# Kernel optimization log

Hardware: AMD Instinct MI355X
Metric: run time of the kernel (lower is better)

Reference implementation:

```python
import jax, jax.numpy as jnp
import numpy as np

H = 256
V = 10000
E = 300000


def setup_inputs() -> dict:
    key = jax.random.key(0)
    ks = jax.random.split(key, 7)
    s = 1.0 / np.sqrt(H)  # torch nn.Linear default init scale
    x = jax.random.normal(ks[0], (V, H), dtype=jnp.float32)
    e = jax.random.normal(ks[1], (E, H), dtype=jnp.float32)
    edge_index = jax.random.randint(ks[2], (2, E), 0, V, dtype=jnp.int64)
    Us_w = jax.random.uniform(ks[3], (H, H), dtype=jnp.float32, minval=-s, maxval=s)
    Us_b = jax.random.uniform(ks[4], (H,), dtype=jnp.float32, minval=-s, maxval=s)
    Vs_w = jax.random.uniform(ks[5], (H, H), dtype=jnp.float32, minval=-s, maxval=s)
    Vs_b = jax.random.uniform(ks[6], (H,), dtype=jnp.float32, minval=-s, maxval=s)
    return {"x": x, "e": e, "edge_index": edge_index,
            "Us_w": Us_w, "Us_b": Us_b, "Vs_w": Vs_w, "Vs_b": Vs_b}


def reference(x, e, edge_index, Us_w, Us_b, Vs_w, Vs_b):
    # Ue = Us(e): (E, H); Vx = Vs(x): (V, H)  [torch Linear: y = x @ W.T + b]
    Ue = jnp.einsum('eh,oh->eo', e, Us_w) + Us_b
    Vx = jnp.einsum('vh,oh->vo', x, Vs_w) + Vs_b
    src, dst = edge_index[0], edge_index[1]
    # gather + add epilogue: e_new = Ue + Vx[src] + Vx[dst]
    e_new = Ue + Vx[src] + Vx[dst]
    return e_new
```

## Files before the change

kernel.cpp:

```cpp
#include <hip/hip_runtime.h>


typedef __bf16 bf16_t;
typedef __bf16 bf16x4 __attribute__((ext_vector_type(4)));
typedef __bf16 bf16x8 __attribute__((ext_vector_type(8)));
typedef float f32x4 __attribute__((ext_vector_type(4)));
typedef float f32x8 __attribute__((ext_vector_type(8)));

#define HDIM 256
#define NV 10000
#define NE 300000

__device__ __forceinline__ void async16(const bf16_t* g, bf16_t* l) {
  __builtin_amdgcn_global_load_lds(
      (const __attribute__((address_space(1))) void*)g,
      (__attribute__((address_space(3))) void*)l, 16, 0, 0);
}

__global__ __launch_bounds__(256) void cvt_weights(
    const float* __restrict__ us, const float* __restrict__ vs,
    bf16_t* __restrict__ us_o, bf16_t* __restrict__ vs_o) {
  const int c = blockIdx.x * 256 + threadIdx.x;
  const int h = c >> 12;
  const int g = (c >> 6) & 63;
  const int ln = c & 63;
  const int n = h * 128 + ((g >> 2) & 1) * 64 + (g & 3) * 16 + (ln & 15);
  const int kb = (g >> 3) * 32 + (ln >> 4) * 8;
  const float* su = us + n * HDIM + kb;
  const float* sv = vs + n * HDIM + kb;
  f32x4 a0 = *(const f32x4*)su, a1 = *(const f32x4*)(su + 4);
  f32x4 b0 = *(const f32x4*)sv, b1 = *(const f32x4*)(sv + 4);
  f32x8 av = {a0[0], a0[1], a0[2], a0[3], a1[0], a1[1], a1[2], a1[3]};
  f32x8 bv = {b0[0], b0[1], b0[2], b0[3], b1[0], b1[1], b1[2], b1[3]};
  *(bf16x8*)(us_o + c * 8) = __builtin_convertvector(av, bf16x8);
  *(bf16x8*)(vs_o + c * 8) = __builtin_convertvector(bv, bf16x8);
}

template <bool FUSED>
__global__ __launch_bounds__(256) void gemm(
    const float* __restrict__ A,
    const bf16_t* __restrict__ Wb,
    const float* __restrict__ bias,
    const int* __restrict__ sIdxG,
    const int* __restrict__ dIdxG,
    const bf16_t* __restrict__ Vx,
    float* __restrict__ outF,
    bf16_t* __restrict__ outB,
    int M) {
  __shared__ __align__(16) char smem[65536];

  const int tid = threadIdx.x;
  const int lane = tid & 63;
  const int wave = tid >> 6;
  const int wm = wave >> 1;
  const int wn = wave & 1;
  const int l15 = lane & 15;
  const int quad = lane >> 4;

  const int n0 = blockIdx.x * 128;
  const int row0 = blockIdx.y * 128;

  const bf16_t* wsHalf = Wb + (size_t)blockIdx.x * 32768;
  bf16_t* lB = (bf16_t*)smem;
#pragma unroll
  for (int i = 0; i < 16; ++i) {
    const int c = tid + i * 256;
    async16(wsHalf + c * 8, lB + c * 8);
  }

  const float* pA[4];
#pragma unroll
  for (int mi = 0; mi < 4; ++mi) {
    int r = row0 + wm * 64 + mi * 16 + l15;
    if (r >= M) r = M - 1;
    pA[mi] = A + (size_t)r * HDIM + quad * 8;
  }

  f32x4 bufA[4][2], bufB[4][2];
#pragma unroll
  for (int mi = 0; mi < 4; ++mi) {
    bufA[mi][0] = *(const f32x4*)(pA[mi] + 0);
    bufA[mi][1] = *(const f32x4*)(pA[mi] + 4);
    bufB[mi][0] = *(const f32x4*)(pA[mi] + 32);
    bufB[mi][1] = *(const f32x4*)(pA[mi] + 36);
  }

  f32x4 acc[4][4];
#pragma unroll
  for (int mi = 0; mi < 4; ++mi)
#pragma unroll
    for (int ni = 0; ni < 4; ++ni) {
      f32x4 z = {0.f, 0.f, 0.f, 0.f};
      acc[mi][ni] = z;
    }

  const int bOff = wn * 4096 + lane * 16;

  __syncthreads();

#pragma unroll 1
  for (int i = 0; i < 4; ++i) {
    const int k0 = i * 64;
    bf16x8 af[4];
#pragma unroll
    for (int mi = 0; mi < 4; ++mi) {
      f32x8 v = {bufA[mi][0][0], bufA[mi][0][1], bufA[mi][0][2], bufA[mi][0][3],
                 bufA[mi][1][0], bufA[mi][1][1], bufA[mi][1][2], bufA[mi][1][3]};
      af[mi] = __builtin_convertvector(v, bf16x8);
    }
    if (i < 3) {
#pragma unroll
      for (int mi = 0; mi < 4; ++mi) {
        bufA[mi][0] = *(const f32x4*)(pA[mi] + k0 + 64);
        bufA[mi][1] = *(const f32x4*)(pA[mi] + k0 + 68);
      }
    }
#pragma unroll
    for (int ni = 0; ni < 4; ++ni) {
      bf16x8 bfr = *(const bf16x8*)(smem + (2 * i) * 8192 + ni * 1024 + bOff);
#pragma unroll
      for (int mi = 0; mi < 4; ++mi)
        acc[mi][ni] = __builtin_amdgcn_mfma_f32_16x16x32_bf16(
            af[mi], bfr, acc[mi][ni], 0, 0, 0);
    }
#pragma unroll
    for (int mi = 0; mi < 4; ++mi) {
      f32x8 v = {bufB[mi][0][0], bufB[mi][0][1], bufB[mi][0][2], bufB[mi][0][3],
                 bufB[mi][1][0], bufB[mi][1][1], bufB[mi][1][2], bufB[mi][1][3]};
      af[mi] = __builtin_convertvector(v, bf16x8);
    }
    if (i < 3) {
#pragma unroll
      for (int mi = 0; mi < 4; ++mi) {
        bufB[mi][0] = *(const f32x4*)(pA[mi] + k0 + 96);
        bufB[mi][1] = *(const f32x4*)(pA[mi] + k0 + 100);
      }
    }
#pragma unroll
    for (int ni = 0; ni < 4; ++ni) {
      bf16x8 bfr =
          *(const bf16x8*)(smem + (2 * i + 1) * 8192 + ni * 1024 + bOff);
#pragma unroll
      for (int mi = 0; mi < 4; ++mi)
        acc[mi][ni] = __builtin_amdgcn_mfma_f32_16x16x32_bf16(
            af[mi], bfr, acc[mi][ni], 0, 0, 0);
    }
  }

  __syncthreads();

  float bcol[4];
#pragma unroll
  for (int ni = 0; ni < 4; ++ni)
    bcol[ni] = bias[n0 + wn * 64 + ni * 16 + l15];

  float* stage = (float*)smem + wave * (16 * 68);
  const int srow = lane >> 2;
  const int scol = (lane & 3) * 4;

#pragma unroll
  for (int mi = 0; mi < 4; ++mi) {
#pragma unroll
    for (int ni = 0; ni < 4; ++ni)
#pragma unroll
      for (int r = 0; r < 4; ++r)
        stage[(quad * 4 + r) * 68 + ni * 16 + l15] = acc[mi][ni][r] + bcol[ni];

    const int rl = wm * 64 + mi * 16 + srow;
    const int row = row0 + rl;
    if (row < M) {
      const float* sp = stage + srow * 68;
      if constexpr (FUSED) {
        const int si = sIdxG[row];
        const int di = dIdxG[row];
        const bf16_t* vs = Vx + (size_t)si * HDIM + n0 + wn * 64;
        const bf16_t* vd = Vx + (size_t)di * HDIM + n0 + wn * 64;
        float* op = outF + (size_t)row * HDIM + n0 + wn * 64;
#pragma unroll
        for (int i = 0; i < 4; ++i) {
          const int c = i * 16 + scol;
          f32x4 a = *(const f32x4*)(sp + c);
          f32x4 sf = __builtin_convertvector(*(const bf16x4*)(vs + c), f32x4);
          f32x4 df = __builtin_convertvector(*(const bf16x4*)(vd + c), f32x4);
          *(f32x4*)(op + c) = a + sf + df;
        }
      } else {
        bf16_t* op = outB + (size_t)row * HDIM + n0 + wn * 64;
#pragma unroll
        for (int i = 0; i < 4; ++i) {
          const int c = i * 16 + scol;
          f32x4 a = *(const f32x4*)(sp + c);
          *(bf16x4*)(op + c) = __builtin_convertvector(a, bf16x4);
        }
      }
    }
  }
}

extern "C" void kernel_launch(void* const* d_in, const int* in_sizes, int n_in,
                              void* d_out, int out_size, void* d_ws,
                              size_t ws_size, hipStream_t stream) {
  const float* x = (const float*)d_in[0];
  const float* e = (const float*)d_in[1];
  const int* edge = (const int*)d_in[2];
  const float* Us_w = (const float*)d_in[3];
  const float* Us_b = (const float*)d_in[4];
  const float* Vs_w = (const float*)d_in[5];
  const float* Vs_b = (const float*)d_in[6];
  float* out = (float*)d_out;

  bf16_t* us_w_b = (bf16_t*)d_ws;
  bf16_t* vs_w_b = (bf16_t*)((char*)d_ws + (128 << 10));
  bf16_t* Vx = (bf16_t*)((char*)d_ws + (256 << 10));

  dim3 blk(256, 1, 1);

  cvt_weights<<<dim3(32, 1, 1), blk, 0, stream>>>(Us_w, Vs_w, us_w_b, vs_w_b);

  dim3 g1(2, (NV + 127) / 128, 1);
  gemm<false><<<g1, blk, 0, stream>>>(x, vs_w_b, Vs_b, nullptr, nullptr,
                                      nullptr, nullptr, Vx, NV);

  dim3 g2(2, (NE + 127) / 128, 1);
  gemm<true><<<g2, blk, 0, stream>>>(e, us_w_b, Us_b, edge, edge + NE, Vx, out,
                                     nullptr, NE);
}
```

Baseline: 662.0 us.

## Restructure GEMM waves to 32x128 tiles with all A loads issued upfront

```diff
diff --git a/kernel.cpp b/kernel.cpp
--- a/kernel.cpp
+++ b/kernel.cpp
@@ -22,10 +22,13 @@
     bf16_t* __restrict__ us_o, bf16_t* __restrict__ vs_o) {
   const int c = blockIdx.x * 256 + threadIdx.x;
   const int h = c >> 12;
-  const int g = (c >> 6) & 63;
-  const int ln = c & 63;
-  const int n = h * 128 + ((g >> 2) & 1) * 64 + (g & 3) * 16 + (ln & 15);
-  const int kb = (g >> 3) * 32 + (ln >> 4) * 8;
+  const int idx = c & 4095;
+  const int g2 = idx >> 6;
+  const int ln = idx & 63;
+  const int ni = g2 & 7;
+  const int ks = g2 >> 3;
+  const int n = h * 128 + ni * 16 + (ln & 15);
+  const int kb = ks * 32 + (ln >> 4) * 8;
   const float* su = us + n * HDIM + kb;
   const float* sv = vs + n * HDIM + kb;
   f32x4 a0 = *(const f32x4*)su, a1 = *(const f32x4*)(su + 4);
@@ -37,7 +40,7 @@
 }
 
 template <bool FUSED>
-__global__ __launch_bounds__(256) void gemm(
+__global__ __launch_bounds__(256, 2) void gemm(
     const float* __restrict__ A,
     const bf16_t* __restrict__ Wb,
     const float* __restrict__ bias,
@@ -52,8 +55,6 @@
   const int tid = threadIdx.x;
   const int lane = tid & 63;
   const int wave = tid >> 6;
-  const int wm = wave >> 1;
-  const int wn = wave & 1;
   const int l15 = lane & 15;
   const int quad = lane >> 4;
 
@@ -68,80 +69,48 @@
     async16(wsHalf + c * 8, lB + c * 8);
   }
 
-  const float* pA[4];
+  const float* pA[2];
 #pragma unroll
-  for (int mi = 0; mi < 4; ++mi) {
-    int r = row0 + wm * 64 + mi * 16 + l15;
+  for (int mi = 0; mi < 2; ++mi) {
+    int r = row0 + wave * 32 + mi * 16 + l15;
     if (r >= M) r = M - 1;
     pA[mi] = A + (size_t)r * HDIM + quad * 8;
   }
+  f32x4 ar[8][2][2];
+#pragma unroll
+  for (int ks = 0; ks < 8; ++ks)
+#pragma unroll
+    for (int mi = 0; mi < 2; ++mi) {
+      ar[ks][mi][0] = *(const f32x4*)(pA[mi] + ks * 32);
+      ar[ks][mi][1] = *(const f32x4*)(pA[mi] + ks * 32 + 4);
+    }
 
-  f32x4 bufA[4][2], bufB[4][2];
+  f32x4 acc[2][8];
 #pragma unroll
-  for (int mi = 0; mi < 4; ++mi) {
-    bufA[mi][0] = *(const f32x4*)(pA[mi] + 0);
-    bufA[mi][1] = *(const f32x4*)(pA[mi] + 4);
-    bufB[mi][0] = *(const f32x4*)(pA[mi] + 32);
-    bufB[mi][1] = *(const f32x4*)(pA[mi] + 36);
-  }
-
-  f32x4 acc[4][4];
+  for (int mi = 0; mi < 2; ++mi)
 #pragma unroll
-  for (int mi = 0; mi < 4; ++mi)
-#pragma unroll
-    for (int ni = 0; ni < 4; ++ni) {
+    for (int ni = 0; ni < 8; ++ni) {
       f32x4 z = {0.f, 0.f, 0.f, 0.f};
       acc[mi][ni] = z;
     }
 
-  const int bOff = wn * 4096 + lane * 16;
-
   __syncthreads();
 
-#pragma unroll 1
-  for (int i = 0; i < 4; ++i) {
-    const int k0 = i * 64;
-    bf16x8 af[4];
 #pragma unroll
-    for (int mi = 0; mi < 4; ++mi) {
-      f32x8 v = {bufA[mi][0][0], bufA[mi][0][1], bufA[mi][0][2], bufA[mi][0][3],
-                 bufA[mi][1][0], bufA[mi][1][1], bufA[mi][1][2], bufA[mi][1][3]};
+  for (int ks = 0; ks < 8; ++ks) {
+    bf16x8 af[2];
+#pragma unroll
+    for (int mi = 0; mi < 2; ++mi) {
+      f32x8 v = {ar[ks][mi][0][0], ar[ks][mi][0][1], ar[ks][mi][0][2],
+                 ar[ks][mi][0][3], ar[ks][mi][1][0], ar[ks][mi][1][1],
+                 ar[ks][mi][1][2], ar[ks][mi][1][3]};
       af[mi] = __builtin_convertvector(v, bf16x8);
     }
-    if (i < 3) {
 #pragma unroll
-      for (int mi = 0; mi < 4; ++mi) {
-        bufA[mi][0] = *(const f32x4*)(pA[mi] + k0 + 64);
-        bufA[mi][1] = *(const f32x4*)(pA[mi] + k0 + 68);
-      }
-    }
+    for (int ni = 0; ni < 8; ++ni) {
+      bf16x8 bfr = *(const bf16x8*)(smem + (ks * 8 + ni) * 1024 + lane * 16);
 #pragma unroll
-    for (int ni = 0; ni < 4; ++ni) {
-      bf16x8 bfr = *(const bf16x8*)(smem + (2 * i) * 8192 + ni * 1024 + bOff);
-#pragma unroll
-      for (int mi = 0; mi < 4; ++mi)
-        acc[mi][ni] = __builtin_amdgcn_mfma_f32_16x16x32_bf16(
-            af[mi], bfr, acc[mi][ni], 0, 0, 0);
-    }
-#pragma unroll
-    for (int mi = 0; mi < 4; ++mi) {
-      f32x8 v = {bufB[mi][0][0], bufB[mi][0][1], bufB[mi][0][2], bufB[mi][0][3],
-                 bufB[mi][1][0], bufB[mi][1][1], bufB[mi][1][2], bufB[mi][1][3]};
-      af[mi] = __builtin_convertvector(v, bf16x8);
-    }
-    if (i < 3) {
-#pragma unroll
-      for (int mi = 0; mi < 4; ++mi) {
-        bufB[mi][0] = *(const f32x4*)(pA[mi] + k0 + 96);
-        bufB[mi][1] = *(const f32x4*)(pA[mi] + k0 + 100);
-      }
-    }
-#pragma unroll
-    for (int ni = 0; ni < 4; ++ni) {
-      bf16x8 bfr =
-          *(const bf16x8*)(smem + (2 * i + 1) * 8192 + ni * 1024 + bOff);
-#pragma unroll
-      for (int mi = 0; mi < 4; ++mi)
+      for (int mi = 0; mi < 2; ++mi)
         acc[mi][ni] = __builtin_amdgcn_mfma_f32_16x16x32_bf16(
             af[mi], bfr, acc[mi][ni], 0, 0, 0);
     }
@@ -149,35 +118,34 @@
 
   __syncthreads();
 
-  float bcol[4];
+  float bcol[8];
 #pragma unroll
-  for (int ni = 0; ni < 4; ++ni)
-    bcol[ni] = bias[n0 + wn * 64 + ni * 16 + l15];
+  for (int ni = 0; ni < 8; ++ni)
+    bcol[ni] = bias[n0 + ni * 16 + l15];
 
-  float* stage = (float*)smem + wave * (16 * 68);
+  float* stage = (float*)smem + wave * (16 * 132);
   const int srow = lane >> 2;
   const int scol = (lane & 3) * 4;
 
 #pragma unroll
-  for (int mi = 0; mi < 4; ++mi) {
+  for (int mi = 0; mi < 2; ++mi) {
 #pragma unroll
-    for (int ni = 0; ni < 4; ++ni)
+    for (int ni = 0; ni < 8; ++ni)
 #pragma unroll
       for (int r = 0; r < 4; ++r)
-        stage[(quad * 4 + r) * 68 + ni * 16 + l15] = acc[mi][ni][r] + bcol[ni];
+        stage[(quad * 4 + r) * 132 + ni * 16 + l15] = acc[mi][ni][r] + bcol[ni];
 
-    const int rl = wm * 64 + mi * 16 + srow;
-    const int row = row0 + rl;
+    const int row = row0 + wave * 32 + mi * 16 + srow;
     if (row < M) {
-      const float* sp = stage + srow * 68;
+      const float* sp = stage + srow * 132;
       if constexpr (FUSED) {
         const int si = sIdxG[row];
         const int di = dIdxG[row];
-        const bf16_t* vs = Vx + (size_t)si * HDIM + n0 + wn * 64;
-        const bf16_t* vd = Vx + (size_t)di * HDIM + n0 + wn * 64;
-        float* op = outF + (size_t)row * HDIM + n0 + wn * 64;
+        const bf16_t* vs = Vx + (size_t)si * HDIM + n0;
+        const bf16_t* vd = Vx + (size_t)di * HDIM + n0;
+        float* op = outF + (size_t)row * HDIM + n0;
 #pragma unroll
-        for (int i = 0; i < 4; ++i) {
+        for (int i = 0; i < 8; ++i) {
           const int c = i * 16 + scol;
           f32x4 a = *(const f32x4*)(sp + c);
           f32x4 sf = __builtin_convertvector(*(const bf16x4*)(vs + c), f32x4);
@@ -185,9 +153,9 @@
           *(f32x4*)(op + c) = a + sf + df;
         }
       } else {
-        bf16_t* op = outB + (size_t)row * HDIM + n0 + wn * 64;
+        bf16_t* op = outB + (size_t)row * HDIM + n0;
 #pragma unroll
-        for (int i = 0; i < 4; ++i) {
+        for (int i = 0; i < 8; ++i) {
           const int c = i * 16 + scol;
           f32x4 a = *(const f32x4*)(sp + c);
           *(bf16x4*)(op + c) = __builtin_convertvector(a, bf16x4);
```

Measured after the change: 563.5 us. -14.9%, faster.
